# Performance work log

Measured on AMD Instinct MI355X. Metric: run time of the kernel, lower is better.

## Reference

```python
import jax, jax.numpy as jnp
import numpy as np

N_NODES = 100000
N_EDGES = 1600000
D_IN = 64
D_OUT = 64
ROW_WINDOW = 16  # TCGNN row-window size (metadata only)


def setup_inputs() -> dict:
    key = jax.random.key(0)
    ks = jax.random.split(key, 7)
    X = jax.random.normal(ks[0], (N_NODES, D_IN), dtype=jnp.float32)
    weights = jax.random.normal(ks[1], (D_IN, D_OUT), dtype=jnp.float32)
    # CSR row pointers: sorted offsets into the edge list, endpoints pinned.
    rp = jnp.sort(jax.random.randint(ks[2], (N_NODES + 1,), 0, N_EDGES, dtype=jnp.int32))
    row_pointers = rp.at[0].set(0).at[-1].set(N_EDGES)
    column_index = jax.random.randint(ks[3], (N_EDGES,), 0, N_NODES, dtype=jnp.int32)
    # TCGNN tiling metadata (does not affect the math; kept for signature fidelity)
    blockPartition = jax.random.randint(ks[4], (N_NODES // ROW_WINDOW,), 0, 8, dtype=jnp.int32)
    edgeToColumn = jax.random.randint(ks[5], (N_EDGES,), 0, N_NODES, dtype=jnp.int32)
    edgeToRow = jax.random.randint(ks[6], (N_EDGES,), 0, N_NODES, dtype=jnp.int32)
    return {
        "X": X,
        "weights": weights,
        "row_pointers": row_pointers,
        "column_index": column_index,
        "blockPartition": blockPartition,
        "edgeToColumn": edgeToColumn,
        "edgeToRow": edgeToRow,
    }


def reference(X, weights, row_pointers, column_index, blockPartition, edgeToColumn, edgeToRow):
    # TCGNN.forward == unweighted CSR SpMM: X_prime[i] = sum_{j in N(i)} X[j]
    n_edges = column_index.shape[0]
    # Map each edge position to its CSR row id.
    row_ids = jnp.searchsorted(row_pointers, jnp.arange(n_edges, dtype=row_pointers.dtype), side="right") - 1
    gathered = X[column_index]  # [n_edges, d_in] irregular gather
    X_prime = jax.ops.segment_sum(gathered, row_ids, num_segments=X.shape[0])  # [n_nodes, d_in]
    return X_prime @ weights  # dense GEMM [n_nodes, d_out]
```

## Files before the change

kernel.cpp:

```cpp
#include <hip/hip_runtime.h>
#include <cstdint>
#include <cstddef>

#define D 64

typedef float f32x4 __attribute__((ext_vector_type(4)));
typedef uint32_t u32x4 __attribute__((ext_vector_type(4)));

__device__ __forceinline__ uint32_t rne_bf16(float f) {
    uint32_t x = __float_as_uint(f);
    return (x + 0x7fffu + ((x >> 16) & 1u)) >> 16;
}
__device__ __forceinline__ float bf16lo(uint32_t u) { return __uint_as_float(u << 16); }
__device__ __forceinline__ float bf16hi(uint32_t u) { return __uint_as_float(u & 0xffff0000u); }

__global__ __launch_bounds__(256) void cast_kernel(
    const float* __restrict__ X, uint32_t* __restrict__ Xh, long n4)
{
    long i = (long)blockIdx.x * blockDim.x + threadIdx.x;
    const long stride = (long)gridDim.x * blockDim.x;
    for (; i < n4; i += stride) {
        f32x4 v = __builtin_nontemporal_load((const f32x4*)X + i);
        uint2 o;
        o.x = rne_bf16(v.x) | (rne_bf16(v.y) << 16);
        o.y = rne_bf16(v.z) | (rne_bf16(v.w) << 16);
        ((uint2*)Xh)[i] = o;
    }
}

__global__ __launch_bounds__(256, 4) void gather_gemm_kernel(
    const uint32_t* __restrict__ Xh, const float* __restrict__ W,
    const int* __restrict__ rp, const int* __restrict__ ci,
    float* __restrict__ out, int n_nodes)
{
    const int lane = threadIdx.x & 63;
    const int o = lane >> 3;
    const int p = lane & 7;

    float wcol[D];
#pragma unroll
    for (int d = 0; d < D; ++d) wcol[d] = W[d * D + lane];

    const int gwave = (int)((blockIdx.x * blockDim.x + threadIdx.x) >> 6);
    const int nwaves = (int)((gridDim.x * blockDim.x) >> 6);

    for (int row = gwave; row < n_nodes; row += nwaves) {
        const int e0 = rp[row];
        const int e1 = rp[row + 1];

        float r[8], s[8];
#pragma unroll
        for (int j = 0; j < 8; ++j) { r[j] = 0.f; s[j] = 0.f; }

        int e = e0;
        for (; e + 16 <= e1; e += 16) {
            const int i0 = ci[e + o];
            const int i1 = ci[e + 8 + o];
            const u32x4 u = *(const u32x4*)(Xh + (size_t)i0 * 32 + p * 4);
            const u32x4 v = *(const u32x4*)(Xh + (size_t)i1 * 32 + p * 4);
#pragma unroll
            for (int k = 0; k < 4; ++k) {
                r[2 * k]     += bf16lo(u[k]);
                r[2 * k + 1] += bf16hi(u[k]);
                s[2 * k]     += bf16lo(v[k]);
                s[2 * k + 1] += bf16hi(v[k]);
            }
        }
        if (e + 8 <= e1) {
            const int i0 = ci[e + o];
            const u32x4 u = *(const u32x4*)(Xh + (size_t)i0 * 32 + p * 4);
#pragma unroll
            for (int k = 0; k < 4; ++k) {
                r[2 * k]     += bf16lo(u[k]);
                r[2 * k + 1] += bf16hi(u[k]);
            }
            e += 8;
        }
        const int rem = e1 - e;
        if (o < rem) {
            const int i0 = ci[e + o];
            const u32x4 u = *(const u32x4*)(Xh + (size_t)i0 * 32 + p * 4);
#pragma unroll
            for (int k = 0; k < 4; ++k) {
                s[2 * k]     += bf16lo(u[k]);
                s[2 * k + 1] += bf16hi(u[k]);
            }
        }

#pragma unroll
        for (int j = 0; j < 8; ++j) r[j] += s[j];
#pragma unroll
        for (int j = 0; j < 8; ++j) {
            r[j] += __shfl_xor(r[j], 8, 64);
            r[j] += __shfl_xor(r[j], 16, 64);
            r[j] += __shfl_xor(r[j], 32, 64);
        }

        float g0 = 0.f, g1 = 0.f, g2 = 0.f, g3 = 0.f;
#pragma unroll
        for (int d = 0; d < D; d += 4) {
            g0 += __int_as_float(__builtin_amdgcn_readlane(__float_as_int(r[(d + 0) & 7]), (d + 0) >> 3)) * wcol[d + 0];
            g1 += __int_as_float(__builtin_amdgcn_readlane(__float_as_int(r[(d + 1) & 7]), (d + 1) >> 3)) * wcol[d + 1];
            g2 += __int_as_float(__builtin_amdgcn_readlane(__float_as_int(r[(d + 2) & 7]), (d + 2) >> 3)) * wcol[d + 2];
            g3 += __int_as_float(__builtin_amdgcn_readlane(__float_as_int(r[(d + 3) & 7]), (d + 3) >> 3)) * wcol[d + 3];
        }
        const float g = (g0 + g1) + (g2 + g3);
        __builtin_nontemporal_store(g, out + (size_t)row * D + lane);
    }
}

__global__ __launch_bounds__(256) void fused_kernel(
    const float* __restrict__ X, const float* __restrict__ W,
    const int* __restrict__ rp, const int* __restrict__ ci,
    float* __restrict__ out, int n_nodes)
{
    __shared__ float Wl[D * D];
    for (int i = threadIdx.x; i < D * D; i += 256) Wl[i] = W[i];
    __syncthreads();

    const int lane = threadIdx.x & 63;
    const int gwave = (int)((blockIdx.x * blockDim.x + threadIdx.x) >> 6);
    const int nwaves = (int)((gridDim.x * blockDim.x) >> 6);

    for (int row = gwave; row < n_nodes; row += nwaves) {
        int e0 = rp[row];
        int e1 = rp[row + 1];
        float acc = 0.f;
        for (int e = e0; e < e1; ++e) acc += X[ci[e] * D + lane];
        float sum = 0.f;
#pragma unroll
        for (int d = 0; d < D; ++d) {
            float a = __shfl(acc, d, 64);
            sum += a * Wl[d * D + lane];
        }
        out[row * D + lane] = sum;
    }
}

extern "C" void kernel_launch(void* const* d_in, const int* in_sizes, int n_in,
                              void* d_out, int out_size, void* d_ws, size_t ws_size,
                              hipStream_t stream)
{
    const float* X  = (const float*)d_in[0];
    const float* W  = (const float*)d_in[1];
    const int*   rp = (const int*)d_in[2];
    const int*   ci = (const int*)d_in[3];
    float* out = (float*)d_out;

    const int n_nodes = in_sizes[2] - 1;
    const size_t xh_bytes = (size_t)n_nodes * 32 * sizeof(uint32_t);

    if (ws_size >= xh_bytes) {
        uint32_t* Xh = (uint32_t*)d_ws;
        const long n4 = (long)n_nodes * (D / 4);
        int cast_blocks = (int)((n4 + 255) / 256);
        if (cast_blocks > 6400) cast_blocks = 6400;
        cast_kernel<<<cast_blocks, 256, 0, stream>>>(X, Xh, n4);
        gather_gemm_kernel<<<2048, 256, 0, stream>>>(Xh, W, rp, ci, out, n_nodes);
    } else {
        fused_kernel<<<2048, 256, 0, stream>>>(X, W, rp, ci, out, n_nodes);
    }
}
```

Before: 167.3 us.

## Split gather and GEMM into separate kernels, using MFMA bf16 for the dense GEMM

The fused gather+scalar-GEMM kernel is replaced by two kernels. The first aggregates two rows per wave with 8-byte loads, 16 lanes per row and 4 edges in flight per row, and writes the aggregates as bf16 to the workspace. The second runs the 64x64 GEMM on 16-row tiles with mfma_f32_16x16x32_bf16, holding W in registers as bf16. This removes the per-row readlane/FMA GEMM cost, but adds an extra launch, an aggregate write and read round trip, and bf16 rounding of both the aggregates and W.

```diff
diff --git a/kernel.cpp b/kernel.cpp
--- a/kernel.cpp
+++ b/kernel.cpp
@@ -4,8 +4,8 @@
 
 #define D 64
 
-typedef float f32x4 __attribute__((ext_vector_type(4)));
-typedef uint32_t u32x4 __attribute__((ext_vector_type(4)));
+typedef float  f32x4 __attribute__((ext_vector_type(4)));
+typedef short  s16x8 __attribute__((ext_vector_type(8)));
 
 __device__ __forceinline__ uint32_t rne_bf16(float f) {
     uint32_t x = __float_as_uint(f);
@@ -28,84 +28,163 @@
     }
 }
 
-__global__ __launch_bounds__(256, 4) void gather_gemm_kernel(
-    const uint32_t* __restrict__ Xh, const float* __restrict__ W,
-    const int* __restrict__ rp, const int* __restrict__ ci,
+__global__ __launch_bounds__(256) void gather2_kernel(
+    const uint32_t* __restrict__ Xh, const int* __restrict__ rp,
+    const int* __restrict__ ci, uint32_t* __restrict__ Agg, int n_nodes)
+{
+    const int lane = threadIdx.x & 63;
+    const int o = lane >> 4;
+    const int p = lane & 15;
+    const int w = (int)((blockIdx.x * blockDim.x + threadIdx.x) >> 6);
+    const int rowA = 2 * w;
+    if (rowA >= n_nodes) return;
+    const int rowB = rowA + 1;
+    const bool hasB = rowB < n_nodes;
+
+    int ea = rp[rowA];
+    const int a1 = rp[rowA + 1];
+    int eb = hasB ? rp[rowB] : 0;
+    const int b1 = hasB ? rp[rowB + 1] : 0;
+
+    float A0[4] = {0,0,0,0}, A1[4] = {0,0,0,0};
+    float B0[4] = {0,0,0,0}, B1[4] = {0,0,0,0};
+
+    for (;;) {
+        const bool da = (ea + 8 <= a1);
+        const bool db = (eb + 8 <= b1);
+        if (!da && !db) break;
+        int ia0, ia1, ib0, ib1;
+        if (da) { ia0 = ci[ea + o]; ia1 = ci[ea + 4 + o]; }
+        if (db) { ib0 = ci[eb + o]; ib1 = ci[eb + 4 + o]; }
+        uint2 ua0, ua1, ub0, ub1;
+        if (da) {
+            ua0 = *(const uint2*)(Xh + (size_t)ia0 * 32 + p * 2);
+            ua1 = *(const uint2*)(Xh + (size_t)ia1 * 32 + p * 2);
+        }
+        if (db) {
+            ub0 = *(const uint2*)(Xh + (size_t)ib0 * 32 + p * 2);
+            ub1 = *(const uint2*)(Xh + (size_t)ib1 * 32 + p * 2);
+        }
+        if (da) {
+            A0[0] += bf16lo(ua0.x); A0[1] += bf16hi(ua0.x); A0[2] += bf16lo(ua0.y); A0[3] += bf16hi(ua0.y);
+            A1[0] += bf16lo(ua1.x); A1[1] += bf16hi(ua1.x); A1[2] += bf16lo(ua1.y); A1[3] += bf16hi(ua1.y);
+            ea += 8;
+        }
+        if (db) {
+            B0[0] += bf16lo(ub0.x); B0[1] += bf16hi(ub0.x); B0[2] += bf16lo(ub0.y); B0[3] += bf16hi(ub0.y);
+            B1[0] += bf16lo(ub1.x); B1[1] += bf16hi(ub1.x); B1[2] += bf16lo(ub1.y); B1[3] += bf16hi(ub1.y);
+            eb += 8;
+        }
+    }
+
+    {
+        const bool da = (ea + 4 <= a1);
+        const bool db = (eb + 4 <= b1);
+        int ia, ib; uint2 ua, ub;
+        if (da) ia = ci[ea + o];
+        if (db) ib = ci[eb + o];
+        if (da) ua = *(const uint2*)(Xh + (size_t)ia * 32 + p * 2);
+        if (db) ub = *(const uint2*)(Xh + (size_t)ib * 32 + p * 2);
+        if (da) {
+            A0[0] += bf16lo(ua.x); A0[1] += bf16hi(ua.x); A0[2] += bf16lo(ua.y); A0[3] += bf16hi(ua.y);
+            ea += 4;
+        }
+        if (db) {
+            B0[0] += bf16lo(ub.x); B0[1] += bf16hi(ub.x); B0[2] += bf16lo(ub.y); B0[3] += bf16hi(ub.y);
+            eb += 4;
+        }
+    }
+    {
+        const int ra = a1 - ea, rb = b1 - eb;
+        const bool dal = (o < ra), dbl = (o < rb);
+        int ia, ib; uint2 ua, ub;
+        if (dal) ia = ci[ea + o];
+        if (dbl) ib = ci[eb + o];
+        if (dal) ua = *(const uint2*)(Xh + (size_t)ia * 32 + p * 2);
+        if (dbl) ub = *(const uint2*)(Xh + (size_t)ib * 32 + p * 2);
+        if (dal) {
+            A1[0] += bf16lo(ua.x); A1[1] += bf16hi(ua.x); A1[2] += bf16lo(ua.y); A1[3] += bf16hi(ua.y);
+        }
+        if (dbl) {
+            B1[0] += bf16lo(ub.x); B1[1] += bf16hi(ub.x); B1[2] += bf16lo(ub.y); B1[3] += bf16hi(ub.y);
+        }
+    }
+
+#pragma unroll
+    for (int j = 0; j < 4; ++j) {
+        float va = A0[j] + A1[j];
+        va += __shfl_xor(va, 16, 64);
+        va += __shfl_xor(va, 32, 64);
+        A0[j] = va;
+        float vb = B0[j] + B1[j];
+        vb += __shfl_xor(vb, 16, 64);
+        vb += __shfl_xor(vb, 32, 64);
+        B0[j] = vb;
+    }
+    if (lane < 16) {
+        uint2 oa;
+        oa.x = rne_bf16(A0[0]) | (rne_bf16(A0[1]) << 16);
+        oa.y = rne_bf16(A0[2]) | (rne_bf16(A0[3]) << 16);
+        *(uint2*)(Agg + (size_t)rowA * 32 + p * 2) = oa;
+        if (hasB) {
+            uint2 ob;
+            ob.x = rne_bf16(B0[0]) | (rne_bf16(B0[1]) << 16);
+            ob.y = rne_bf16(B0[2]) | (rne_bf16(B0[3]) << 16);
+            *(uint2*)(Agg + (size_t)rowB * 32 + p * 2) = ob;
+        }
+    }
+}
+
+__global__ __launch_bounds__(256) void agg_gemm_kernel(
+    const uint32_t* __restrict__ Agg, const float* __restrict__ W,
     float* __restrict__ out, int n_nodes)
 {
     const int lane = threadIdx.x & 63;
-    const int o = lane >> 3;
-    const int p = lane & 7;
-
-    float wcol[D];
-#pragma unroll
-    for (int d = 0; d < D; ++d) wcol[d] = W[d * D + lane];
-
+    const int n = lane & 15;
+    const int q = lane >> 4;
+
+    s16x8 Bf[4][2];
+#pragma unroll
+    for (int c = 0; c < 4; ++c)
+#pragma unroll
+        for (int kb = 0; kb < 2; ++kb) {
+            s16x8 b;
+#pragma unroll
+            for (int j = 0; j < 8; ++j) {
+                const int k = kb * 32 + q * 8 + j;
+                b[j] = (short)rne_bf16(W[k * D + c * 16 + n]);
+            }
+            Bf[c][kb] = b;
+        }
+
+    const int n_tiles = (n_nodes + 15) / 16;
     const int gwave = (int)((blockIdx.x * blockDim.x + threadIdx.x) >> 6);
     const int nwaves = (int)((gridDim.x * blockDim.x) >> 6);
 
-    for (int row = gwave; row < n_nodes; row += nwaves) {
-        const int e0 = rp[row];
-        const int e1 = rp[row + 1];
-
-        float r[8], s[8];
-#pragma unroll
-        for (int j = 0; j < 8; ++j) { r[j] = 0.f; s[j] = 0.f; }
-
-        int e = e0;
-        for (; e + 16 <= e1; e += 16) {
-            const int i0 = ci[e + o];
-            const int i1 = ci[e + 8 + o];
-            const u32x4 u = *(const u32x4*)(Xh + (size_t)i0 * 32 + p * 4);
-            const u32x4 v = *(const u32x4*)(Xh + (size_t)i1 * 32 + p * 4);
-#pragma unroll
-            for (int k = 0; k < 4; ++k) {
-                r[2 * k]     += bf16lo(u[k]);
-                r[2 * k + 1] += bf16hi(u[k]);
-                s[2 * k]     += bf16lo(v[k]);
-                s[2 * k + 1] += bf16hi(v[k]);
+    for (int t = gwave; t < n_tiles; t += nwaves) {
+        const int m0 = t * 16;
+        int arow = m0 + n;
+        if (arow >= n_nodes) arow = n_nodes - 1;
+        const s16x8 A0 = *(const s16x8*)(Agg + (size_t)arow * 32 + q * 4);
+        const s16x8 A1 = *(const s16x8*)(Agg + (size_t)arow * 32 + 16 + q * 4);
+
+        f32x4 acc[4];
+#pragma unroll
+        for (int c = 0; c < 4; ++c) {
+            f32x4 z = {0.f, 0.f, 0.f, 0.f};
+            z = __builtin_amdgcn_mfma_f32_16x16x32_bf16(A0, Bf[c][0], z, 0, 0, 0);
+            z = __builtin_amdgcn_mfma_f32_16x16x32_bf16(A1, Bf[c][1], z, 0, 0, 0);
+            acc[c] = z;
+        }
+#pragma unroll
+        for (int r = 0; r < 4; ++r) {
+            const int ro = m0 + q * 4 + r;
+            if (ro < n_nodes) {
+#pragma unroll
+                for (int c = 0; c < 4; ++c)
+                    out[(size_t)ro * D + c * 16 + n] = acc[c][r];
             }
         }
-        if (e + 8 <= e1) {
-            const int i0 = ci[e + o];
-            const u32x4 u = *(const u32x4*)(Xh + (size_t)i0 * 32 + p * 4);
-#pragma unroll
-            for (int k = 0; k < 4; ++k) {
-                r[2 * k]     += bf16lo(u[k]);
-                r[2 * k + 1] += bf16hi(u[k]);
-            }
-            e += 8;
-        }
-        const int rem = e1 - e;
-        if (o < rem) {
-            const int i0 = ci[e + o];
-            const u32x4 u = *(const u32x4*)(Xh + (size_t)i0 * 32 + p * 4);
-#pragma unroll
-            for (int k = 0; k < 4; ++k) {
-                s[2 * k]     += bf16lo(u[k]);
-                s[2 * k + 1] += bf16hi(u[k]);
-            }
-        }
-
-#pragma unroll
-        for (int j = 0; j < 8; ++j) r[j] += s[j];
-#pragma unroll
-        for (int j = 0; j < 8; ++j) {
-            r[j] += __shfl_xor(r[j], 8, 64);
-            r[j] += __shfl_xor(r[j], 16, 64);
-            r[j] += __shfl_xor(r[j], 32, 64);
-        }
-
-        float g0 = 0.f, g1 = 0.f, g2 = 0.f, g3 = 0.f;
-#pragma unroll
-        for (int d = 0; d < D; d += 4) {
-            g0 += __int_as_float(__builtin_amdgcn_readlane(__float_as_int(r[(d + 0) & 7]), (d + 0) >> 3)) * wcol[d + 0];
-            g1 += __int_as_float(__builtin_amdgcn_readlane(__float_as_int(r[(d + 1) & 7]), (d + 1) >> 3)) * wcol[d + 1];
-            g2 += __int_as_float(__builtin_amdgcn_readlane(__float_as_int(r[(d + 2) & 7]), (d + 2) >> 3)) * wcol[d + 2];
-            g3 += __int_as_float(__builtin_amdgcn_readlane(__float_as_int(r[(d + 3) & 7]), (d + 3) >> 3)) * wcol[d + 3];
-        }
-        const float g = (g0 + g1) + (g2 + g3);
-        __builtin_nontemporal_store(g, out + (size_t)row * D + lane);
     }
 }
 
@@ -148,15 +227,24 @@
     float* out = (float*)d_out;
 
     const int n_nodes = in_sizes[2] - 1;
-    const size_t xh_bytes = (size_t)n_nodes * 32 * sizeof(uint32_t);
-
-    if (ws_size >= xh_bytes) {
-        uint32_t* Xh = (uint32_t*)d_ws;
+    const size_t row_bytes = 32 * sizeof(uint32_t);
+    const size_t need = 2 * (size_t)n_nodes * row_bytes;
+
+    if (ws_size >= need) {
+        uint32_t* Xh  = (uint32_t*)d_ws;
+        uint32_t* Agg = (uint32_t*)((char*)d_ws + (size_t)n_nodes * row_bytes);
+
         const long n4 = (long)n_nodes * (D / 4);
         int cast_blocks = (int)((n4 + 255) / 256);
         if (cast_blocks > 6400) cast_blocks = 6400;
         cast_kernel<<<cast_blocks, 256, 0, stream>>>(X, Xh, n4);
-        gather_gemm_kernel<<<2048, 256, 0, stream>>>(Xh, W, rp, ci, out, n_nodes);
+
+        const int gather_blocks = (((n_nodes + 1) / 2) + 3) / 4;
+        gather2_kernel<<<gather_blocks, 256, 0, stream>>>(Xh, rp, ci, Agg, n_nodes);
+
+        const int n_tiles = (n_nodes + 15) / 16;
+        const int gemm_blocks = (n_tiles + 3) / 4;
+        agg_gemm_kernel<<<gemm_blocks, 256, 0, stream>>>(Agg, W, out, n_nodes);
     } else {
         fused_kernel<<<2048, 256, 0, stream>>>(X, W, rp, ci, out, n_nodes);
     }
```

New measurement: 154.4 us. 7.7% less time.

## Split gather and GEMM into separate kernels, using MFMA bf16 for the GEMM

Applied to the files above, without the earlier changes.

Replaces the fused gather-plus-scalar-GEMM kernel with two kernels. The first is a one-wave-per-row gather with a deeper unroll (32 edges per iteration) that writes bf16 aggregates to workspace. The second computes the dense projection with MFMA 16x16x32 bf16 instructions over 16-row tiles. This is meant to remove the per-row readlane/FMA GEMM cost and the register pressure from holding a W column in every lane. In exchange it adds a kernel launch, an extra bf16 round trip through memory for the aggregates, and extra rounding of both the aggregate and W to bf16.

```diff
diff --git a/kernel.cpp b/kernel.cpp
--- a/kernel.cpp
+++ b/kernel.cpp
@@ -4,7 +4,8 @@
 
 #define D 64
 
-typedef float f32x4 __attribute__((ext_vector_type(4)));
+typedef float    f32x4 __attribute__((ext_vector_type(4)));
+typedef short    s16x8 __attribute__((ext_vector_type(8)));
 typedef uint32_t u32x4 __attribute__((ext_vector_type(4)));
 
 __device__ __forceinline__ uint32_t rne_bf16(float f) {
@@ -28,84 +29,137 @@
     }
 }
 
-__global__ __launch_bounds__(256, 4) void gather_gemm_kernel(
-    const uint32_t* __restrict__ Xh, const float* __restrict__ W,
-    const int* __restrict__ rp, const int* __restrict__ ci,
-    float* __restrict__ out, int n_nodes)
+__global__ __launch_bounds__(256) void gather3_kernel(
+    const uint32_t* __restrict__ Xh, const int* __restrict__ rp,
+    const int* __restrict__ ci, uint32_t* __restrict__ Agg, int n_nodes)
 {
     const int lane = threadIdx.x & 63;
     const int o = lane >> 3;
     const int p = lane & 7;
-
-    float wcol[D];
-#pragma unroll
-    for (int d = 0; d < D; ++d) wcol[d] = W[d * D + lane];
-
+    const int row = (int)((blockIdx.x * blockDim.x + threadIdx.x) >> 6);
+    if (row >= n_nodes) return;
+
+    const int e0 = rp[row];
+    const int e1 = rp[row + 1];
+
+    float a[8] = {0,0,0,0,0,0,0,0};
+    float b[8] = {0,0,0,0,0,0,0,0};
+
+    int e = e0;
+    for (; e + 32 <= e1; e += 32) {
+        const int i0 = ci[e      + o];
+        const int i1 = ci[e +  8 + o];
+        const int i2 = ci[e + 16 + o];
+        const int i3 = ci[e + 24 + o];
+        const u32x4 u0 = *(const u32x4*)(Xh + (size_t)i0 * 32 + p * 4);
+        const u32x4 u1 = *(const u32x4*)(Xh + (size_t)i1 * 32 + p * 4);
+        const u32x4 u2 = *(const u32x4*)(Xh + (size_t)i2 * 32 + p * 4);
+        const u32x4 u3 = *(const u32x4*)(Xh + (size_t)i3 * 32 + p * 4);
+#pragma unroll
+        for (int k = 0; k < 4; ++k) {
+            a[2*k] += bf16lo(u0[k]); a[2*k+1] += bf16hi(u0[k]);
+            b[2*k] += bf16lo(u1[k]); b[2*k+1] += bf16hi(u1[k]);
+            a[2*k] += bf16lo(u2[k]); a[2*k+1] += bf16hi(u2[k]);
+            b[2*k] += bf16lo(u3[k]); b[2*k+1] += bf16hi(u3[k]);
+        }
+    }
+    if (e + 16 <= e1) {
+        const int i0 = ci[e     + o];
+        const int i1 = ci[e + 8 + o];
+        const u32x4 u0 = *(const u32x4*)(Xh + (size_t)i0 * 32 + p * 4);
+        const u32x4 u1 = *(const u32x4*)(Xh + (size_t)i1 * 32 + p * 4);
+#pragma unroll
+        for (int k = 0; k < 4; ++k) {
+            a[2*k] += bf16lo(u0[k]); a[2*k+1] += bf16hi(u0[k]);
+            b[2*k] += bf16lo(u1[k]); b[2*k+1] += bf16hi(u1[k]);
+        }
+        e += 16;
+    }
+    if (e + 8 <= e1) {
+        const int i0 = ci[e + o];
+        const u32x4 u0 = *(const u32x4*)(Xh + (size_t)i0 * 32 + p * 4);
+#pragma unroll
+        for (int k = 0; k < 4; ++k) {
+            a[2*k] += bf16lo(u0[k]); a[2*k+1] += bf16hi(u0[k]);
+        }
+        e += 8;
+    }
+    if (o < e1 - e) {
+        const int i0 = ci[e + o];
+        const u32x4 u0 = *(const u32x4*)(Xh + (size_t)i0 * 32 + p * 4);
+#pragma unroll
+        for (int k = 0; k < 4; ++k) {
+            b[2*k] += bf16lo(u0[k]); b[2*k+1] += bf16hi(u0[k]);
+        }
+    }
+
+#pragma unroll
+    for (int j = 0; j < 8; ++j) {
+        float v = a[j] + b[j];
+        v += __shfl_xor(v, 8, 64);
+        v += __shfl_xor(v, 16, 64);
+        v += __shfl_xor(v, 32, 64);
+        a[j] = v;
+    }
+    if (lane < 8) {
+        u32x4 w;
+#pragma unroll
+        for (int k = 0; k < 4; ++k)
+            w[k] = rne_bf16(a[2*k]) | (rne_bf16(a[2*k+1]) << 16);
+        *(u32x4*)(Agg + (size_t)row * 32 + p * 4) = w;
+    }
+}
+
+__global__ __launch_bounds__(256) void agg_gemm_kernel(
+    const uint32_t* __restrict__ Agg, const float* __restrict__ W,
+    float* __restrict__ out, int n_nodes)
+{
+    const int lane = threadIdx.x & 63;
+    const int n = lane & 15;
+    const int q = lane >> 4;
+
+    s16x8 Bf[4][2];
+#pragma unroll
+    for (int c = 0; c < 4; ++c)
+#pragma unroll
+        for (int kb = 0; kb < 2; ++kb) {
+            s16x8 bfr;
+#pragma unroll
+            for (int j = 0; j < 8; ++j) {
+                const int k = kb * 32 + q * 8 + j;
+                bfr[j] = (short)rne_bf16(W[k * D + c * 16 + n]);
+            }
+            Bf[c][kb] = bfr;
+        }
+
+    const int n_tiles = (n_nodes + 15) / 16;
     const int gwave = (int)((blockIdx.x * blockDim.x + threadIdx.x) >> 6);
     const int nwaves = (int)((gridDim.x * blockDim.x) >> 6);
 
-    for (int row = gwave; row < n_nodes; row += nwaves) {
-        const int e0 = rp[row];
-        const int e1 = rp[row + 1];
-
-        float r[8], s[8];
-#pragma unroll
-        for (int j = 0; j < 8; ++j) { r[j] = 0.f; s[j] = 0.f; }
-
-        int e = e0;
-        for (; e + 16 <= e1; e += 16) {
-            const int i0 = ci[e + o];
-            const int i1 = ci[e + 8 + o];
-            const u32x4 u = *(const u32x4*)(Xh + (size_t)i0 * 32 + p * 4);
-            const u32x4 v = *(const u32x4*)(Xh + (size_t)i1 * 32 + p * 4);
-#pragma unroll
-            for (int k = 0; k < 4; ++k) {
-                r[2 * k]     += bf16lo(u[k]);
-                r[2 * k + 1] += bf16hi(u[k]);
-                s[2 * k]     += bf16lo(v[k]);
-                s[2 * k + 1] += bf16hi(v[k]);
+    for (int t = gwave; t < n_tiles; t += nwaves) {
+        const int m0 = t * 16;
+        int arow = m0 + n;
+        if (arow >= n_nodes) arow = n_nodes - 1;
+        const s16x8 A0 = *(const s16x8*)(Agg + (size_t)arow * 32 + q * 4);
+        const s16x8 A1 = *(const s16x8*)(Agg + (size_t)arow * 32 + 16 + q * 4);
+
+        f32x4 acc[4];
+#pragma unroll
+        for (int c = 0; c < 4; ++c) {
+            f32x4 z = {0.f, 0.f, 0.f, 0.f};
+            z = __builtin_amdgcn_mfma_f32_16x16x32_bf16(A0, Bf[c][0], z, 0, 0, 0);
+            z = __builtin_amdgcn_mfma_f32_16x16x32_bf16(A1, Bf[c][1], z, 0, 0, 0);
+            acc[c] = z;
+        }
+#pragma unroll
+        for (int r = 0; r < 4; ++r) {
+            const int ro = m0 + q * 4 + r;
+            if (ro < n_nodes) {
+#pragma unroll
+                for (int c = 0; c < 4; ++c)
+                    out[(size_t)ro * D + c * 16 + n] = acc[c][r];
             }
         }
-        if (e + 8 <= e1) {
-            const int i0 = ci[e + o];
-            const u32x4 u = *(const u32x4*)(Xh + (size_t)i0 * 32 + p * 4);
-#pragma unroll
-            for (int k = 0; k < 4; ++k) {
-                r[2 * k]     += bf16lo(u[k]);
-                r[2 * k + 1] += bf16hi(u[k]);
-            }
-            e += 8;
-        }
-        const int rem = e1 - e;
-        if (o < rem) {
-            const int i0 = ci[e + o];
-            const u32x4 u = *(const u32x4*)(Xh + (size_t)i0 * 32 + p * 4);
-#pragma unroll
-            for (int k = 0; k < 4; ++k) {
-                s[2 * k]     += bf16lo(u[k]);
-                s[2 * k + 1] += bf16hi(u[k]);
-            }
-        }
-
-#pragma unroll
-        for (int j = 0; j < 8; ++j) r[j] += s[j];
-#pragma unroll
-        for (int j = 0; j < 8; ++j) {
-            r[j] += __shfl_xor(r[j], 8, 64);
-            r[j] += __shfl_xor(r[j], 16, 64);
-            r[j] += __shfl_xor(r[j], 32, 64);
-        }
-
-        float g0 = 0.f, g1 = 0.f, g2 = 0.f, g3 = 0.f;
-#pragma unroll
-        for (int d = 0; d < D; d += 4) {
-            g0 += __int_as_float(__builtin_amdgcn_readlane(__float_as_int(r[(d + 0) & 7]), (d + 0) >> 3)) * wcol[d + 0];
-            g1 += __int_as_float(__builtin_amdgcn_readlane(__float_as_int(r[(d + 1) & 7]), (d + 1) >> 3)) * wcol[d + 1];
-            g2 += __int_as_float(__builtin_amdgcn_readlane(__float_as_int(r[(d + 2) & 7]), (d + 2) >> 3)) * wcol[d + 2];
-            g3 += __int_as_float(__builtin_amdgcn_readlane(__float_as_int(r[(d + 3) & 7]), (d + 3) >> 3)) * wcol[d + 3];
-        }
-        const float g = (g0 + g1) + (g2 + g3);
-        __builtin_nontemporal_store(g, out + (size_t)row * D + lane);
     }
 }
 
@@ -148,15 +202,24 @@
     float* out = (float*)d_out;
 
     const int n_nodes = in_sizes[2] - 1;
-    const size_t xh_bytes = (size_t)n_nodes * 32 * sizeof(uint32_t);
-
-    if (ws_size >= xh_bytes) {
-        uint32_t* Xh = (uint32_t*)d_ws;
+    const size_t row_bytes = 32 * sizeof(uint32_t);
+    const size_t need = 2 * (size_t)n_nodes * row_bytes;
+
+    if (ws_size >= need) {
+        uint32_t* Xh  = (uint32_t*)d_ws;
+        uint32_t* Agg = (uint32_t*)((char*)d_ws + (size_t)n_nodes * row_bytes);
+
         const long n4 = (long)n_nodes * (D / 4);
         int cast_blocks = (int)((n4 + 255) / 256);
         if (cast_blocks > 6400) cast_blocks = 6400;
         cast_kernel<<<cast_blocks, 256, 0, stream>>>(X, Xh, n4);
-        gather_gemm_kernel<<<2048, 256, 0, stream>>>(Xh, W, rp, ci, out, n_nodes);
+
+        const int gather_blocks = (n_nodes + 3) / 4;
+        gather3_kernel<<<gather_blocks, 256, 0, stream>>>(Xh, rp, ci, Agg, n_nodes);
+
+        const int n_tiles = (n_nodes + 15) / 16;
+        const int gemm_blocks = (n_tiles + 3) / 4;
+        agg_gemm_kernel<<<gemm_blocks, 256, 0, stream>>>(Agg, W, out, n_nodes);
     } else {
         fused_kernel<<<2048, 256, 0, stream>>>(X, W, rp, ci, out, n_nodes);
     }
```

Result: faster. 146.3 us (-12.6%).
